# Kernel tuning notes

Measured on AMD Instinct MI355X. Metric: run time of the kernel, lower is better.

## Reference

```python
import jax, jax.numpy as jnp
import numpy as np

B, N, C = 8, 1024, 768
H = 12
HD = C // H  # 64
SCALE = C ** (-0.5)  # NOTE: source scales by n_emb^-0.5, not head_dim^-0.5


def setup_inputs() -> dict:
    key = jax.random.key(0)
    k1, k2, k3 = jax.random.split(key, 3)
    x = jax.random.normal(k1, (B, N, C), dtype=jnp.float32)
    W_qkv = jax.random.normal(k2, (C, 3 * C), dtype=jnp.float32) * (C ** -0.5)
    b_qkv = jnp.zeros((3 * C,), dtype=jnp.float32)
    W_proj = jax.random.normal(k3, (C, C), dtype=jnp.float32) * (C ** -0.5)
    b_proj = jnp.zeros((C,), dtype=jnp.float32)
    return {"x": x, "W_qkv": W_qkv, "b_qkv": b_qkv, "W_proj": W_proj, "b_proj": b_proj}


def reference(x, W_qkv, b_qkv, W_proj, b_proj):
    # qkv projection: (B,N,3C) -> (3,B,H,N,HD)
    qkv = x @ W_qkv + b_qkv
    qkv = qkv.reshape(B, N, 3, H, HD).transpose(2, 0, 3, 1, 4)
    q, k, v = qkv[0], qkv[1], qkv[2]
    # scaled dot-product attention (full N x N, as in source)
    attn = jnp.einsum("bhnd,bhmd->bhnm", q, k) * SCALE
    attn = jax.nn.softmax(attn, axis=-1)
    out = jnp.einsum("bhnm,bhmd->bhnd", attn, v)
    out = out.transpose(0, 2, 1, 3).reshape(B, N, C)
    return out @ W_proj + b_proj
```

## Files before the change

### kernel.cpp

```cpp
#include <hip/hip_runtime.h>
#include <hip/hip_bf16.h>
#include <stdint.h>

#define Bb 8
#define Nn_ 1024
#define Cc_ 768
#define Hh 12
#define HDd 64
#define BHh 96
#define SCALE_F 0.03608439182435161f
#define CL2F (0.03608439182435161f * 1.4426950408889634f)
#define THRRAW (3.0f / CL2F)

typedef __attribute__((ext_vector_type(4))) float f32x4;
typedef __attribute__((ext_vector_type(8))) __bf16 bf16x8;

__device__ __forceinline__ unsigned short f2bf(float f) {
  uint32_t u = __builtin_bit_cast(uint32_t, f);
  uint32_t r = (u + 0x7fffu + ((u >> 16) & 1u)) >> 16;
  return (unsigned short)r;
}

__device__ __forceinline__ uint32_t cvtpk(float a, float b) {
  uint32_t r;
  asm("v_cvt_pk_bf16_f32 %0, %1, %2" : "=v"(r) : "v"(a), "v"(b));
  return r;
}

__device__ __forceinline__ f32x4 mfma16(bf16x8 a, bf16x8 b, f32x4 c) {
  return __builtin_amdgcn_mfma_f32_16x16x32_bf16(a, b, c, 0, 0, 0);
}

typedef const __attribute__((address_space(1))) uint32_t* gas1_t;
typedef __attribute__((address_space(3))) uint32_t* las3_t;
__device__ __forceinline__ void gl_lds16(const void* g, void* l) {
  __builtin_amdgcn_global_load_lds((gas1_t)g, (las3_t)l, 16, 0, 0);
}

__global__ void k_cvt_x(const float* __restrict__ x, unsigned short* __restrict__ xb, int n4) {
  int i = blockIdx.x * blockDim.x + threadIdx.x;
  if (i >= n4) return;
  float4 v = ((const float4*)x)[i];
  ushort4 o;
  o.x = f2bf(v.x); o.y = f2bf(v.y); o.z = f2bf(v.z); o.w = f2bf(v.w);
  ((ushort4*)xb)[i] = o;
}

template <int R, int CC>
__global__ void k_transpose(const float* __restrict__ src, unsigned short* __restrict__ dst) {
  __shared__ unsigned short tile[64][65];
  int c0 = blockIdx.x * 64;
  int r0 = blockIdx.y * 64;
  int t = threadIdx.x;
#pragma unroll
  for (int i = 0; i < 16; ++i) {
    int idx = t + 256 * i;
    int r = idx >> 6, c = idx & 63;
    tile[r][c] = f2bf(src[(size_t)(r0 + r) * CC + c0 + c]);
  }
  __syncthreads();
#pragma unroll
  for (int i = 0; i < 16; ++i) {
    int idx = t + 256 * i;
    int a = idx >> 6, bq = idx & 63;
    dst[(size_t)(c0 + a) * R + r0 + bq] = tile[bq][a];
  }
}

__global__ __launch_bounds__(256) void k_transpose_v(const unsigned short* __restrict__ V,
                                                     unsigned short* __restrict__ Vt) {
  __shared__ unsigned short tile[64][72];
  int bh = blockIdx.y;
  int n0 = blockIdx.x * 64;
  int t = threadIdx.x;
  const unsigned short* src = V + ((size_t)bh * 1024 + n0) * 64;
#pragma unroll
  for (int i = 0; i < 4; ++i) {
    int idx = t + i * 256;
    int r = idx >> 4, c4 = idx & 15;
    ushort4 v = ((const ushort4*)src)[idx];
    tile[r][c4 * 4 + 0] = v.x; tile[r][c4 * 4 + 1] = v.y;
    tile[r][c4 * 4 + 2] = v.z; tile[r][c4 * 4 + 3] = v.w;
  }
  __syncthreads();
  unsigned short* dst = Vt + (size_t)bh * 64 * 1024 + n0;
#pragma unroll
  for (int i = 0; i < 4; ++i) {
    int idx = t + i * 256;
    int c = idx >> 4, n4 = idx & 15;
    ushort4 o;
    o.x = tile[n4 * 4 + 0][c]; o.y = tile[n4 * 4 + 1][c];
    o.z = tile[n4 * 4 + 2][c]; o.w = tile[n4 * 4 + 3][c];
    ((ushort4*)(dst + (size_t)c * 1024))[n4] = o;
  }
}

#define BM 128
#define BN 128

template <int EPI>
__global__ __launch_bounds__(256, 2) void k_gemm(
    const unsigned short* __restrict__ A, const unsigned short* __restrict__ Bt,
    const float* __restrict__ bias, float* __restrict__ out,
    unsigned short* __restrict__ Qb, unsigned short* __restrict__ Kb,
    unsigned short* __restrict__ Vb, int M, int Nw, int K) {
  __shared__ char smem[2][32768];
  int t = threadIdx.x;
  int w = t >> 6, lane = t & 63;
  int g = lane >> 4, l15 = lane & 15;
  int m0 = blockIdx.x * BM;
  int n0 = blockIdx.y * BN;
  int wr = w >> 1, wc = w & 1;

  f32x4 acc[4][4] = {};

  int soff[4], srow[4], ssb[4];
#pragma unroll
  for (int it = 0; it < 4; ++it) {
    int off = it * 4096 + t * 16;
    soff[it] = it * 4096 + w * 1024;
    srow[it] = off >> 7;
    ssb[it] = (off & 127) ^ ((srow[it] & 7) << 4);
  }

  auto STAGE = [&](int buf, int kt) {
    int k0 = kt * 64;
    char* As = smem[buf];
    char* Bs = smem[buf] + 16384;
#pragma unroll
    for (int it = 0; it < 4; ++it)
      gl_lds16(&A[(size_t)(m0 + srow[it]) * K + k0 + (ssb[it] >> 1)], As + soff[it]);
#pragma unroll
    for (int it = 0; it < 4; ++it)
      gl_lds16(&Bt[(size_t)(n0 + srow[it]) * K + k0 + (ssb[it] >> 1)], Bs + soff[it]);
  };

  STAGE(0, 0);
  __syncthreads();

  int nkt = K >> 6;
  for (int kt = 0; kt < nkt; ++kt) {
    int cur = kt & 1;
    if (kt + 1 < nkt) STAGE(cur ^ 1, kt + 1);
    char* As = smem[cur];
    char* Bs = smem[cur] + 16384;
    bf16x8 av[2][4], bv[2][4];
#pragma unroll
    for (int ks = 0; ks < 2; ++ks) {
      int kb = ks * 64 + g * 16;
#pragma unroll
      for (int mi = 0; mi < 4; ++mi) {
        int row = wr * 64 + mi * 16 + l15;
        av[ks][mi] = *(const bf16x8*)(As + row * 128 + (kb ^ ((row & 7) << 4)));
      }
#pragma unroll
      for (int ni = 0; ni < 4; ++ni) {
        int row = wc * 64 + ni * 16 + l15;
        bv[ks][ni] = *(const bf16x8*)(Bs + row * 128 + (kb ^ ((row & 7) << 4)));
      }
    }
#pragma unroll
    for (int ks = 0; ks < 2; ++ks)
#pragma unroll
      for (int mi = 0; mi < 4; ++mi)
#pragma unroll
        for (int ni = 0; ni < 4; ++ni)
          acc[mi][ni] = mfma16(av[ks][mi], bv[ks][ni], acc[mi][ni]);
    __syncthreads();
  }

#pragma unroll
  for (int mi = 0; mi < 4; ++mi) {
#pragma unroll
    for (int ni = 0; ni < 4; ++ni) {
      int col = n0 + wc * 64 + ni * 16 + l15;
      float bvs = bias[col];
#pragma unroll
      for (int j = 0; j < 4; ++j) {
        int row = m0 + wr * 64 + mi * 16 + g * 4 + j;
        float val = acc[mi][ni][j] + bvs;
        if constexpr (EPI == 0) {
          out[(size_t)row * Nw + col] = val;
        } else {
          int bI = row >> 10, n = row & 1023;
          int typ = col / 768, within = col % 768;
          int h = within >> 6, d = within & 63;
          int bh = bI * 12 + h;
          unsigned short bf = f2bf(val);
          unsigned short* dst = (typ == 0) ? Qb : (typ == 1) ? Kb : Vb;
          dst[((size_t)bh * 1024 + n) * 64 + d] = bf;
        }
      }
    }
  }
}

__global__ __launch_bounds__(256, 3) void k_attn(
    const unsigned short* __restrict__ Q, const unsigned short* __restrict__ K,
    const unsigned short* __restrict__ Vt, unsigned short* __restrict__ Oa) {
  __shared__ char smem[49152];
  char* Ks = smem;
  char* Vs = smem + 16384;
  char* Ps = smem + 32768;
  int t = threadIdx.x, w = t >> 6, lane = t & 63;
  int g = lane >> 4, l15 = lane & 15;
  int n0 = blockIdx.x * 128;
  int bh = blockIdx.y;
  int bI = bh / 12, h = bh % 12;
  char* Pw = Ps + w * 4096;

  bf16x8 qf[2][2];
  {
    const char* qbase = (const char*)Q + ((size_t)bh * 1024 + n0 + w * 32 + l15) * 128 + g * 16;
    qf[0][0] = *(const bf16x8*)(qbase);
    qf[0][1] = *(const bf16x8*)(qbase + 64);
    qf[1][0] = *(const bf16x8*)(qbase + 16 * 128);
    qf[1][1] = *(const bf16x8*)(qbase + 16 * 128 + 64);
  }

  f32x4 acc[2][4] = {};
  float mrun[2] = {-INFINITY, -INFINITY};
  float lrun[2] = {0.f, 0.f};

  int o0 = t * 16, o1 = t * 16 + 4096;
  int r0 = o0 >> 7, r1 = o1 >> 7;
  int sb0 = (o0 & 127) ^ ((r0 & 7) << 4);
  int sb1 = (o1 & 127) ^ ((r1 & 7) << 4);
  const char* Kg = (const char*)K + ((size_t)bh * 1024) * 128;
  const char* Vg = (const char*)Vt + ((size_t)bh * 64) * 2048;

  gl_lds16(Kg + (size_t)r0 * 128 + sb0, Ks + w * 1024);
  gl_lds16(Kg + (size_t)r1 * 128 + sb1, Ks + 4096 + w * 1024);
  gl_lds16(Vg + (size_t)r0 * 2048 + sb0, Vs + w * 1024);
  gl_lds16(Vg + (size_t)r1 * 2048 + sb1, Vs + 4096 + w * 1024);
  __syncthreads();

  for (int mt = 0; mt < 16; ++mt) {
    int cur = mt & 1;
    char* Kc = Ks + cur * 8192;
    char* Vc = Vs + cur * 8192;
    if (mt < 15) {
      int m1 = (mt + 1) * 64;
      char* Kn = Ks + (cur ^ 1) * 8192;
      char* Vn = Vs + (cur ^ 1) * 8192;
      gl_lds16(Kg + (size_t)(m1 + r0) * 128 + sb0, Kn + w * 1024);
      gl_lds16(Kg + (size_t)(m1 + r1) * 128 + sb1, Kn + 4096 + w * 1024);
      gl_lds16(Vg + (size_t)r0 * 2048 + m1 * 2 + sb0, Vn + w * 1024);
      gl_lds16(Vg + (size_t)r1 * 2048 + m1 * 2 + sb1, Vn + 4096 + w * 1024);
    }

    f32x4 s[4][2] = {};
#pragma unroll
    for (int ks = 0; ks < 2; ++ks) {
#pragma unroll
      for (int f = 0; f < 4; ++f) {
        int row = f * 16 + l15;
        bf16x8 kv = *(const bf16x8*)(Kc + row * 128 + ((ks * 64 + g * 16) ^ ((row & 7) << 4)));
        s[f][0] = mfma16(kv, qf[0][ks], s[f][0]);
        s[f][1] = mfma16(kv, qf[1][ks], s[f][1]);
      }
    }

    float pmax[2];
#pragma unroll
    for (int q = 0; q < 2; ++q) {
      float a0 = fmaxf(fmaxf(s[0][q][0], s[0][q][1]), fmaxf(s[0][q][2], s[0][q][3]));
      float a1 = fmaxf(fmaxf(s[1][q][0], s[1][q][1]), fmaxf(s[1][q][2], s[1][q][3]));
      float a2 = fmaxf(fmaxf(s[2][q][0], s[2][q][1]), fmaxf(s[2][q][2], s[2][q][3]));
      float a3 = fmaxf(fmaxf(s[3][q][0], s[3][q][1]), fmaxf(s[3][q][2], s[3][q][3]));
      float pm = fmaxf(fmaxf(a0, a1), fmaxf(a2, a3));
      pm = fmaxf(pm, __shfl_xor(pm, 16, 64));
      pm = fmaxf(pm, __shfl_xor(pm, 32, 64));
      pmax[q] = pm;
    }

    bool upd = (pmax[0] > mrun[0] + THRRAW) || (pmax[1] > mrun[1] + THRRAW);
    if (__any(upd)) {
#pragma unroll
      for (int q = 0; q < 2; ++q) {
        float mnew = fmaxf(mrun[q], pmax[q]);
        float alpha = __builtin_amdgcn_exp2f((mrun[q] - mnew) * CL2F);
        mrun[q] = mnew;
        lrun[q] *= alpha;
#pragma unroll
        for (int j = 0; j < 4; ++j) {
          float aj = __shfl(alpha, g * 4 + j, 64);
          acc[q][0][j] *= aj; acc[q][1][j] *= aj;
          acc[q][2][j] *= aj; acc[q][3][j] *= aj;
        }
      }
    }

#pragma unroll
    for (int q = 0; q < 2; ++q) {
      float nm = -mrun[q] * CL2F;
      int prow = q * 16 + l15;
      int pbase = prow * 128;
      int swz = (prow & 7) << 4;
      float rs = 0.f;
#pragma unroll
      for (int f = 0; f < 4; ++f) {
        float p0 = __builtin_amdgcn_exp2f(fmaf(s[f][q][0], CL2F, nm));
        float p1 = __builtin_amdgcn_exp2f(fmaf(s[f][q][1], CL2F, nm));
        float p2 = __builtin_amdgcn_exp2f(fmaf(s[f][q][2], CL2F, nm));
        float p3 = __builtin_amdgcn_exp2f(fmaf(s[f][q][3], CL2F, nm));
        rs += (p0 + p1) + (p2 + p3);
        uint2 pk;
        pk.x = cvtpk(p0, p1);
        pk.y = cvtpk(p2, p3);
        *(uint2*)(Pw + pbase + ((f * 32 + g * 8) ^ swz)) = pk;
      }
      rs += __shfl_xor(rs, 16, 64);
      rs += __shfl_xor(rs, 32, 64);
      lrun[q] += rs;
    }

#pragma unroll
    for (int ks = 0; ks < 2; ++ks) {
      bf16x8 pa[2];
#pragma unroll
      for (int q = 0; q < 2; ++q) {
        int prow = q * 16 + l15;
        pa[q] = *(const bf16x8*)(Pw + prow * 128 + ((ks * 64 + g * 16) ^ ((prow & 7) << 4)));
      }
#pragma unroll
      for (int fd = 0; fd < 4; ++fd) {
        int vrow = fd * 16 + l15;
        bf16x8 vv = *(const bf16x8*)(Vc + vrow * 128 + ((ks * 64 + g * 16) ^ ((vrow & 7) << 4)));
        acc[0][fd] = mfma16(pa[0], vv, acc[0][fd]);
        acc[1][fd] = mfma16(pa[1], vv, acc[1][fd]);
      }
    }
    __syncthreads();
  }

#pragma unroll
  for (int q = 0; q < 2; ++q) {
#pragma unroll
    for (int j = 0; j < 4; ++j) {
      float lv = __shfl(lrun[q], g * 4 + j, 64);
      float inv = 1.0f / lv;
      int n = n0 + w * 32 + q * 16 + g * 4 + j;
      size_t rowb = ((size_t)bI * 1024 + n) * 768 + h * 64;
#pragma unroll
      for (int fd = 0; fd < 4; ++fd)
        Oa[rowb + fd * 16 + l15] = (unsigned short)(cvtpk(acc[q][fd][j] * inv, 0.f) & 0xffffu);
    }
  }
}

extern "C" void kernel_launch(void* const* d_in, const int* in_sizes, int n_in,
                              void* d_out, int out_size, void* d_ws, size_t ws_size,
                              hipStream_t stream) {
  const float* x = (const float*)d_in[0];
  const float* Wqkv = (const float*)d_in[1];
  const float* bqkv = (const float*)d_in[2];
  const float* Wproj = (const float*)d_in[3];
  const float* bproj = (const float*)d_in[4];
  float* out = (float*)d_out;

  char* ws = (char*)d_ws;
  unsigned short* xb  = (unsigned short*)(ws);
  unsigned short* wqt = (unsigned short*)(ws + 12582912);
  unsigned short* wpt = (unsigned short*)(ws + 16121856);
  unsigned short* Qb  = (unsigned short*)(ws + 17301504);
  unsigned short* Kb  = (unsigned short*)(ws + 29884416);
  unsigned short* Vtb = (unsigned short*)(ws + 42467328);
  unsigned short* Oa  = (unsigned short*)(ws + 55050240);
  unsigned short* Vb  = Oa;

  k_cvt_x<<<dim3(6144), dim3(256), 0, stream>>>(x, xb, (Bb * Nn_ * Cc_) / 4);
  k_transpose<768, 2304><<<dim3(36, 12), dim3(256), 0, stream>>>(Wqkv, wqt);
  k_transpose<768, 768><<<dim3(12, 12), dim3(256), 0, stream>>>(Wproj, wpt);
  k_gemm<1><<<dim3(64, 18), dim3(256), 0, stream>>>(xb, wqt, bqkv, nullptr, Qb, Kb, Vb,
                                                    8192, 2304, 768);
  k_transpose_v<<<dim3(16, 96), dim3(256), 0, stream>>>(Vb, Vtb);
  k_attn<<<dim3(8, 96), dim3(256), 0, stream>>>(Qb, Kb, Vtb, Oa);
  k_gemm<0><<<dim3(64, 6), dim3(256), 0, stream>>>(Oa, wpt, bproj, out, nullptr, nullptr, nullptr,
                                                   8192, 768, 768);
}
```

Measured before the change: 119.2 us.

## Pipeline GEMM and attention loads with explicit vmcnt waits and block remapping

Both the GEMM and attention kernels now wait on global-to-LDS copies with explicit s_waitcnt vmcnt counts and raw s_barrier plus sched_barrier fences instead of __syncthreads. The aim is to keep the next tile's prefetch in flight while the current tile is computed. K is hardcoded to 768 and the GEMM loop is fully unrolled over 12 tiles with precomputed global and LDS pointers, cutting per-iteration address arithmetic. The attention grid becomes 1D with a remapped block index, intended to change L2 locality and scheduling order. The risks are fragile manual wait counts and the loss of generality in K.

```diff
diff --git a/kernel.cpp b/kernel.cpp
--- a/kernel.cpp
+++ b/kernel.cpp
@@ -37,6 +37,10 @@
   __builtin_amdgcn_global_load_lds((gas1_t)g, (las3_t)l, 16, 0, 0);
 }
 
+#define VMCNT(n) asm volatile("s_waitcnt vmcnt(" #n ")" ::: "memory")
+#define SBAR() __builtin_amdgcn_s_barrier()
+#define SCHED_FENCE() __builtin_amdgcn_sched_barrier(0)
+
 __global__ void k_cvt_x(const float* __restrict__ x, unsigned short* __restrict__ xb, int n4) {
   int i = blockIdx.x * blockDim.x + threadIdx.x;
   if (i >= n4) return;
@@ -103,7 +107,7 @@
     const unsigned short* __restrict__ A, const unsigned short* __restrict__ Bt,
     const float* __restrict__ bias, float* __restrict__ out,
     unsigned short* __restrict__ Qb, unsigned short* __restrict__ Kb,
-    unsigned short* __restrict__ Vb, int M, int Nw, int K) {
+    unsigned short* __restrict__ Vb, int M, int Nw) {
   __shared__ char smem[2][32768];
   int t = threadIdx.x;
   int w = t >> 6, lane = t & 63;
@@ -114,51 +118,50 @@
 
   f32x4 acc[4][4] = {};
 
-  int soff[4], srow[4], ssb[4];
+  int soff[4];
+  const char* gA[4];
+  const char* gB[4];
 #pragma unroll
   for (int it = 0; it < 4; ++it) {
     int off = it * 4096 + t * 16;
     soff[it] = it * 4096 + w * 1024;
-    srow[it] = off >> 7;
-    ssb[it] = (off & 127) ^ ((srow[it] & 7) << 4);
-  }
-
-  auto STAGE = [&](int buf, int kt) {
-    int k0 = kt * 64;
+    int row = off >> 7;
+    int sb = (off & 127) ^ ((row & 7) << 4);
+    gA[it] = (const char*)A + (size_t)(m0 + row) * 1536 + sb;
+    gB[it] = (const char*)Bt + (size_t)(n0 + row) * 1536 + sb;
+  }
+
+  auto STG = [&](int buf, int kt) {
     char* As = smem[buf];
     char* Bs = smem[buf] + 16384;
 #pragma unroll
-    for (int it = 0; it < 4; ++it)
-      gl_lds16(&A[(size_t)(m0 + srow[it]) * K + k0 + (ssb[it] >> 1)], As + soff[it]);
-#pragma unroll
-    for (int it = 0; it < 4; ++it)
-      gl_lds16(&Bt[(size_t)(n0 + srow[it]) * K + k0 + (ssb[it] >> 1)], Bs + soff[it]);
+    for (int it = 0; it < 4; ++it) gl_lds16(gA[it] + kt * 128, As + soff[it]);
+#pragma unroll
+    for (int it = 0; it < 4; ++it) gl_lds16(gB[it] + kt * 128, Bs + soff[it]);
   };
 
-  STAGE(0, 0);
-  __syncthreads();
-
-  int nkt = K >> 6;
-  for (int kt = 0; kt < nkt; ++kt) {
-    int cur = kt & 1;
-    if (kt + 1 < nkt) STAGE(cur ^ 1, kt + 1);
-    char* As = smem[cur];
-    char* Bs = smem[cur] + 16384;
+  const char *pa[2][4], *pb[2][4];
+#pragma unroll
+  for (int ks = 0; ks < 2; ++ks) {
+    int kb = ks * 64 + g * 16;
+#pragma unroll
+    for (int mi = 0; mi < 4; ++mi) {
+      int rowA = wr * 64 + mi * 16 + l15;
+      pa[ks][mi] = smem[0] + rowA * 128 + (kb ^ ((rowA & 7) << 4));
+      int rowB = wc * 64 + mi * 16 + l15;
+      pb[ks][mi] = smem[0] + 16384 + rowB * 128 + (kb ^ ((rowB & 7) << 4));
+    }
+  }
+
+  auto CMP = [&](int off) {
     bf16x8 av[2][4], bv[2][4];
 #pragma unroll
-    for (int ks = 0; ks < 2; ++ks) {
-      int kb = ks * 64 + g * 16;
+    for (int ks = 0; ks < 2; ++ks)
 #pragma unroll
       for (int mi = 0; mi < 4; ++mi) {
-        int row = wr * 64 + mi * 16 + l15;
-        av[ks][mi] = *(const bf16x8*)(As + row * 128 + (kb ^ ((row & 7) << 4)));
-      }
-#pragma unroll
-      for (int ni = 0; ni < 4; ++ni) {
-        int row = wc * 64 + ni * 16 + l15;
-        bv[ks][ni] = *(const bf16x8*)(Bs + row * 128 + (kb ^ ((row & 7) << 4)));
-      }
-    }
+        av[ks][mi] = *(const bf16x8*)(pa[ks][mi] + off);
+        bv[ks][mi] = *(const bf16x8*)(pb[ks][mi] + off);
+      }
 #pragma unroll
     for (int ks = 0; ks < 2; ++ks)
 #pragma unroll
@@ -166,7 +169,23 @@
 #pragma unroll
         for (int ni = 0; ni < 4; ++ni)
           acc[mi][ni] = mfma16(av[ks][mi], bv[ks][ni], acc[mi][ni]);
-    __syncthreads();
+  };
+
+  STG(0, 0);
+#pragma unroll
+  for (int kt = 0; kt < 12; ++kt) {
+    int cur = kt & 1;
+    if (kt < 11) {
+      STG(cur ^ 1, kt + 1);
+      VMCNT(8);
+    } else {
+      VMCNT(0);
+    }
+    SBAR();
+    SCHED_FENCE();
+    CMP(cur * 32768);
+    SCHED_FENCE();
+    if (kt < 11) SBAR();
   }
 
 #pragma unroll
@@ -200,12 +219,13 @@
     const unsigned short* __restrict__ Vt, unsigned short* __restrict__ Oa) {
   __shared__ char smem[49152];
   char* Ks = smem;
-  char* Vs = smem + 16384;
   char* Ps = smem + 32768;
   int t = threadIdx.x, w = t >> 6, lane = t & 63;
   int g = lane >> 4, l15 = lane & 15;
-  int n0 = blockIdx.x * 128;
-  int bh = blockIdx.y;
+
+  int fb = blockIdx.x;
+  int bh = (fb & 7) * 12 + ((fb >> 3) % 12);
+  int n0 = (fb / 96) * 128;
   int bI = bh / 12, h = bh % 12;
   char* Pw = Ps + w * 4096;
 
@@ -222,44 +242,53 @@
   float mrun[2] = {-INFINITY, -INFINITY};
   float lrun[2] = {0.f, 0.f};
 
+  const char* pK[2][4];
+#pragma unroll
+  for (int ks = 0; ks < 2; ++ks)
+#pragma unroll
+    for (int ff = 0; ff < 4; ++ff) {
+      int row = ff * 16 + l15;
+      pK[ks][ff] = Ks + row * 128 + ((ks * 64 + g * 16) ^ ((row & 7) << 4));
+    }
+  char* pPw[2][4];
+  const char* pPr[2][2];
+#pragma unroll
+  for (int q = 0; q < 2; ++q) {
+    int prow = q * 16 + l15, swz = (l15 & 7) << 4;
+#pragma unroll
+    for (int ff = 0; ff < 4; ++ff) pPw[q][ff] = Pw + prow * 128 + ((ff * 32 + g * 8) ^ swz);
+#pragma unroll
+    for (int ks = 0; ks < 2; ++ks) pPr[q][ks] = Pw + prow * 128 + ((ks * 64 + g * 16) ^ swz);
+  }
+
   int o0 = t * 16, o1 = t * 16 + 4096;
   int r0 = o0 >> 7, r1 = o1 >> 7;
   int sb0 = (o0 & 127) ^ ((r0 & 7) << 4);
   int sb1 = (o1 & 127) ^ ((r1 & 7) << 4);
-  const char* Kg = (const char*)K + ((size_t)bh * 1024) * 128;
-  const char* Vg = (const char*)Vt + ((size_t)bh * 64) * 2048;
-
-  gl_lds16(Kg + (size_t)r0 * 128 + sb0, Ks + w * 1024);
-  gl_lds16(Kg + (size_t)r1 * 128 + sb1, Ks + 4096 + w * 1024);
-  gl_lds16(Vg + (size_t)r0 * 2048 + sb0, Vs + w * 1024);
-  gl_lds16(Vg + (size_t)r1 * 2048 + sb1, Vs + 4096 + w * 1024);
-  __syncthreads();
-
-  for (int mt = 0; mt < 16; ++mt) {
-    int cur = mt & 1;
-    char* Kc = Ks + cur * 8192;
-    char* Vc = Vs + cur * 8192;
-    if (mt < 15) {
-      int m1 = (mt + 1) * 64;
-      char* Kn = Ks + (cur ^ 1) * 8192;
-      char* Vn = Vs + (cur ^ 1) * 8192;
-      gl_lds16(Kg + (size_t)(m1 + r0) * 128 + sb0, Kn + w * 1024);
-      gl_lds16(Kg + (size_t)(m1 + r1) * 128 + sb1, Kn + 4096 + w * 1024);
-      gl_lds16(Vg + (size_t)r0 * 2048 + m1 * 2 + sb0, Vn + w * 1024);
-      gl_lds16(Vg + (size_t)r1 * 2048 + m1 * 2 + sb1, Vn + 4096 + w * 1024);
-    }
-
+  const char* KgA = (const char*)K + (size_t)bh * 131072 + (size_t)r0 * 128 + sb0;
+  const char* KgB = (const char*)K + (size_t)bh * 131072 + (size_t)r1 * 128 + sb1;
+  const char* VgA = (const char*)Vt + (size_t)bh * 131072 + (size_t)r0 * 2048 + sb0;
+  const char* VgB = (const char*)Vt + (size_t)bh * 131072 + (size_t)r1 * 2048 + sb1;
+
+  auto STG = [&](int buf, int mt) {
+    char* Kd = Ks + buf * 8192;
+    char* Vd = Ks + 16384 + buf * 8192;
+    gl_lds16(KgA + (size_t)mt * 8192, Kd + w * 1024);
+    gl_lds16(KgB + (size_t)mt * 8192, Kd + 4096 + w * 1024);
+    gl_lds16(VgA + (size_t)mt * 128, Vd + w * 1024);
+    gl_lds16(VgB + (size_t)mt * 128, Vd + 4096 + w * 1024);
+  };
+
+  auto TILE = [&](int off) {
     f32x4 s[4][2] = {};
 #pragma unroll
-    for (int ks = 0; ks < 2; ++ks) {
-#pragma unroll
-      for (int f = 0; f < 4; ++f) {
-        int row = f * 16 + l15;
-        bf16x8 kv = *(const bf16x8*)(Kc + row * 128 + ((ks * 64 + g * 16) ^ ((row & 7) << 4)));
-        s[f][0] = mfma16(kv, qf[0][ks], s[f][0]);
-        s[f][1] = mfma16(kv, qf[1][ks], s[f][1]);
-      }
-    }
+    for (int ks = 0; ks < 2; ++ks)
+#pragma unroll
+      for (int ff = 0; ff < 4; ++ff) {
+        bf16x8 kv = *(const bf16x8*)(pK[ks][ff] + off);
+        s[ff][0] = mfma16(kv, qf[0][ks], s[ff][0]);
+        s[ff][1] = mfma16(kv, qf[1][ks], s[ff][1]);
+      }
 
     float pmax[2];
 #pragma unroll
@@ -294,21 +323,18 @@
 #pragma unroll
     for (int q = 0; q < 2; ++q) {
       float nm = -mrun[q] * CL2F;
-      int prow = q * 16 + l15;
-      int pbase = prow * 128;
-      int swz = (prow & 7) << 4;
       float rs = 0.f;
 #pragma unroll
-      for (int f = 0; f < 4; ++f) {
-        float p0 = __builtin_amdgcn_exp2f(fmaf(s[f][q][0], CL2F, nm));
-        float p1 = __builtin_amdgcn_exp2f(fmaf(s[f][q][1], CL2F, nm));
-        float p2 = __builtin_amdgcn_exp2f(fmaf(s[f][q][2], CL2F, nm));
-        float p3 = __builtin_amdgcn_exp2f(fmaf(s[f][q][3], CL2F, nm));
+      for (int ff = 0; ff < 4; ++ff) {
+        float p0 = __builtin_amdgcn_exp2f(fmaf(s[ff][q][0], CL2F, nm));
+        float p1 = __builtin_amdgcn_exp2f(fmaf(s[ff][q][1], CL2F, nm));
+        float p2 = __builtin_amdgcn_exp2f(fmaf(s[ff][q][2], CL2F, nm));
+        float p3 = __builtin_amdgcn_exp2f(fmaf(s[ff][q][3], CL2F, nm));
         rs += (p0 + p1) + (p2 + p3);
         uint2 pk;
         pk.x = cvtpk(p0, p1);
         pk.y = cvtpk(p2, p3);
-        *(uint2*)(Pw + pbase + ((f * 32 + g * 8) ^ swz)) = pk;
+        *(uint2*)(pPw[q][ff]) = pk;
       }
       rs += __shfl_xor(rs, 16, 64);
       rs += __shfl_xor(rs, 32, 64);
@@ -317,21 +343,37 @@
 
 #pragma unroll
     for (int ks = 0; ks < 2; ++ks) {
-      bf16x8 pa[2];
-#pragma unroll
-      for (int q = 0; q < 2; ++q) {
-        int prow = q * 16 + l15;
-        pa[q] = *(const bf16x8*)(Pw + prow * 128 + ((ks * 64 + g * 16) ^ ((prow & 7) << 4)));
-      }
+      bf16x8 pa0 = *(const bf16x8*)(pPr[0][ks]);
+      bf16x8 pa1 = *(const bf16x8*)(pPr[1][ks]);
 #pragma unroll
       for (int fd = 0; fd < 4; ++fd) {
-        int vrow = fd * 16 + l15;
-        bf16x8 vv = *(const bf16x8*)(Vc + vrow * 128 + ((ks * 64 + g * 16) ^ ((vrow & 7) << 4)));
-        acc[0][fd] = mfma16(pa[0], vv, acc[0][fd]);
-        acc[1][fd] = mfma16(pa[1], vv, acc[1][fd]);
-      }
-    }
-    __syncthreads();
+        bf16x8 vv = *(const bf16x8*)(pK[ks][fd] + 16384 + off);
+        acc[0][fd] = mfma16(pa0, vv, acc[0][fd]);
+        acc[1][fd] = mfma16(pa1, vv, acc[1][fd]);
+      }
+    }
+  };
+
+  STG(0, 0);
+  for (int mt2 = 0; mt2 < 8; ++mt2) {
+    STG(1, 2 * mt2 + 1);
+    VMCNT(4);
+    SBAR();
+    SCHED_FENCE();
+    TILE(0);
+    SCHED_FENCE();
+    SBAR();
+    if (mt2 < 7) {
+      STG(0, 2 * mt2 + 2);
+      VMCNT(4);
+    } else {
+      VMCNT(0);
+    }
+    SBAR();
+    SCHED_FENCE();
+    TILE(8192);
+    SCHED_FENCE();
+    if (mt2 < 7) SBAR();
   }
 
 #pragma unroll
@@ -373,9 +415,9 @@
   k_transpose<768, 2304><<<dim3(36, 12), dim3(256), 0, stream>>>(Wqkv, wqt);
   k_transpose<768, 768><<<dim3(12, 12), dim3(256), 0, stream>>>(Wproj, wpt);
   k_gemm<1><<<dim3(64, 18), dim3(256), 0, stream>>>(xb, wqt, bqkv, nullptr, Qb, Kb, Vb,
-                                                    8192, 2304, 768);
+                                                    8192, 2304);
   k_transpose_v<<<dim3(16, 96), dim3(256), 0, stream>>>(Vb, Vtb);
-  k_attn<<<dim3(8, 96), dim3(256), 0, stream>>>(Qb, Kb, Vtb, Oa);
+  k_attn<<<dim3(768), dim3(256), 0, stream>>>(Qb, Kb, Vtb, Oa);
   k_gemm<0><<<dim3(64, 6), dim3(256), 0, stream>>>(Oa, wpt, bproj, out, nullptr, nullptr, nullptr,
-                                                   8192, 768, 768);
-}
+                                                   8192, 768);
+}
```

Result: faster. 114.1 us (-4.3%).
